# Kernel optimization log

Measured on AMD Instinct MI355X. Metric: run time of the kernel, lower is better.

## Reference

```python
import jax, jax.numpy as jnp
import numpy as np

B, N, G = 8, 512, 16          # images, proposals/img, gt boxes/img
C = 91                        # num classes (incl background)
FEAT = 256 * 7 * 7            # pooled RoI feature dim = 12544
REP = 1024                    # TwoMLPHead representation size
FG, BG = 0.5, 0.5             # fg/bg IoU thresholds
BBOX_W = (10.0, 10.0, 5.0, 5.0)
BETA = 1.0 / 9.0              # smooth-L1 beta


def setup_inputs() -> dict:
    key = jax.random.key(0)
    ks = jax.random.split(key, 12)
    # valid xyxy boxes inside an ~800x800 image
    tl = jax.random.uniform(ks[0], (B, N, 2), minval=0.0, maxval=700.0)
    wh = jax.random.uniform(ks[1], (B, N, 2), minval=8.0, maxval=128.0)
    proposals = jnp.concatenate([tl, tl + wh], axis=-1)
    gtl = jax.random.uniform(ks[2], (B, G, 2), minval=0.0, maxval=700.0)
    gwh = jax.random.uniform(ks[3], (B, G, 2), minval=8.0, maxval=128.0)
    gt_boxes = jnp.concatenate([gtl, gtl + gwh], axis=-1)
    gt_labels = jax.random.randint(ks[4], (B, G), 1, C)  # foreground labels 1..C-1
    P = N + G
    features = jax.random.normal(ks[5], (B * P, FEAT), dtype=jnp.float32)
    s = 0.01
    return {
        'proposals': proposals, 'gt_boxes': gt_boxes, 'features': features,
        'W1': jax.random.normal(ks[6], (FEAT, REP), jnp.float32) * s,
        'b1': jnp.zeros((REP,), jnp.float32),
        'W2': jax.random.normal(ks[7], (REP, REP), jnp.float32) * s,
        'b2': jnp.zeros((REP,), jnp.float32),
        'Wcls': jax.random.normal(ks[8], (REP, C), jnp.float32) * s,
        'bcls': jnp.zeros((C,), jnp.float32),
        'Wbox': jax.random.normal(ks[9], (REP, C * 4), jnp.float32) * s,
        'bbox': jnp.zeros((C * 4,), jnp.float32),
        'gt_labels': gt_labels,
    }


def _box_iou(gt, pr):
    # gt: [B,G,4], pr: [B,P,4] -> [B,G,P]
    area_g = (gt[..., 2] - gt[..., 0]) * (gt[..., 3] - gt[..., 1])
    area_p = (pr[..., 2] - pr[..., 0]) * (pr[..., 3] - pr[..., 1])
    lt = jnp.maximum(gt[:, :, None, :2], pr[:, None, :, :2])
    rb = jnp.minimum(gt[:, :, None, 2:], pr[:, None, :, 2:])
    wh = jnp.clip(rb - lt, 0.0)
    inter = wh[..., 0] * wh[..., 1]
    return inter / (area_g[:, :, None] + area_p[:, None, :] - inter)


def _encode(ref, gt):
    # torchvision BoxCoder.encode_single; ref/gt: [...,4]
    wx, wy, ww, wh = BBOX_W
    ew = ref[..., 2] - ref[..., 0]; eh = ref[..., 3] - ref[..., 1]
    ex = ref[..., 0] + 0.5 * ew;    ey = ref[..., 1] + 0.5 * eh
    gw = gt[..., 2] - gt[..., 0];   gh = gt[..., 3] - gt[..., 1]
    gx = gt[..., 0] + 0.5 * gw;     gy = gt[..., 1] + 0.5 * gh
    return jnp.stack([
        wx * (gx - ex) / ew, wy * (gy - ey) / eh,
        ww * jnp.log(gw / ew), wh * jnp.log(gh / eh)], axis=-1)


def reference(proposals, gt_boxes, features, W1, b1, W2, b2, Wcls, bcls, Wbox, bbox, gt_labels):
    # add_gt_proposals
    props = jnp.concatenate([proposals, gt_boxes], axis=1)  # [B,P,4]
    # assign_targets_to_proposals (Matcher, allow_low_quality_matches=False)
    iou = _box_iou(gt_boxes, props)                          # [B,G,P]
    matched_vals = iou.max(axis=1)                           # [B,P]
    matched_idx = iou.argmax(axis=1)                         # [B,P]
    labels = jnp.take_along_axis(gt_labels, matched_idx, axis=1)
    labels = jnp.where(matched_vals < BG, 0, labels)                         # background
    labels = jnp.where((matched_vals >= BG) & (matched_vals < FG), -1, labels)  # ignore
    matched_gt = jnp.take_along_axis(gt_boxes, matched_idx[..., None], axis=1)  # [B,P,4]
    reg_targets = _encode(props, matched_gt).reshape(-1, 4)  # [R,4]
    labels = labels.reshape(-1)                               # [R]

    # TwoMLPHead + FastRCNNPredictor
    x = jax.nn.relu(features @ W1 + b1)
    x = jax.nn.relu(x @ W2 + b2)
    class_logits = x @ Wcls + bcls                            # [R,C]
    box_regression = (x @ Wbox + bbox).reshape(-1, C, 4)      # [R,C,4]

    # fastrcnn_loss (all proposals; ignored labels (-1) masked from CE)
    R = class_logits.shape[0]
    valid = (labels >= 0).astype(class_logits.dtype)
    safe_lab = jnp.clip(labels, 0, C - 1)
    logp = jax.nn.log_softmax(class_logits, axis=-1)
    nll = -jnp.take_along_axis(logp, safe_lab[:, None], axis=1)[:, 0]
    classification_loss = (nll * valid).sum() / jnp.maximum(valid.sum(), 1.0)

    pos = (labels > 0).astype(class_logits.dtype)
    pred = jnp.take_along_axis(box_regression, safe_lab[:, None, None], axis=1)[:, 0]  # [R,4]
    d = jnp.abs(pred - reg_targets)
    sl1 = jnp.where(d < BETA, 0.5 * d * d / BETA, d - 0.5 * BETA).sum(-1)
    box_loss = (sl1 * pos).sum() / R

    return jnp.stack([classification_loss, box_loss])
```

## Files before the change

kernel.cpp:

```cpp
#include <hip/hip_runtime.h>
#include <cstdint>
#include <cstddef>

#define BQ   8
#define NP   512
#define GQ   16
#define PP   528
#define RT   4224
#define MPAD 4352
#define CC   91
#define FEATD 12544
#define REPD 1024
#define NH   512
#define NHU  455
#define BETA (1.0f/9.0f)
#define WSC  64.0f

typedef float f32x4 __attribute__((ext_vector_type(4)));
typedef int   v8i  __attribute__((ext_vector_type(8)));
typedef float v16f __attribute__((ext_vector_type(16)));

__device__ __forceinline__ unsigned short f2bf(float f) {
  unsigned int x = __float_as_uint(f);
  unsigned int r = (x + 0x7fffu + ((x >> 16) & 1u)) >> 16;
  return (unsigned short)r;
}
__device__ __forceinline__ float bf2f(unsigned short u) {
  return __uint_as_float((unsigned int)u << 16);
}

__device__ __forceinline__ void ld_lds16(const void* g, void* l) {
  __builtin_amdgcn_global_load_lds(
      (const __attribute__((address_space(1))) void*)g,
      (__attribute__((address_space(3))) void*)l, 16, 0, 0);
}

__device__ __forceinline__ size_t img_off(int row, int kb, int KT) {
  return (size_t)((row >> 7) * KT + (kb >> 6)) * 8192
       + (size_t)((((row >> 5) & 3) << 11) + (((kb >> 4) & 3) << 9)
                  + ((row & 31) << 4) + (kb & 15));
}

constexpr size_t O_W1T = 0;
constexpr size_t SZ_W1T = (size_t)FEATD * REPD;
constexpr size_t O_W2T = O_W1T + SZ_W1T;
constexpr size_t SZ_W2T = (size_t)REPD * REPD;
constexpr size_t O_WH  = O_W2T + SZ_W2T;
constexpr size_t SZ_WH = (size_t)NH * REPD;
constexpr size_t O_BH  = O_WH + SZ_WH;
constexpr size_t SZ_BH = (size_t)NH * 4;
constexpr size_t O_X1  = O_BH + SZ_BH;
constexpr size_t SZ_X1 = (size_t)MPAD * REPD;
constexpr size_t O_X2  = O_X1 + SZ_X1;
constexpr size_t O_LAB = O_X2 + SZ_X1;
constexpr size_t O_TGT = O_LAB + (size_t)RT * 4;
constexpr size_t O_NLL = O_TGT + (size_t)RT * 16;
constexpr size_t O_VC  = O_NLL + (size_t)RT * 4;
constexpr size_t O_SL1 = O_VC + (size_t)RT * 4;
constexpr size_t O_PART = ((O_SL1 + (size_t)RT * 4) + 255) & ~(size_t)255;
constexpr size_t SZ_PART = (size_t)4 * MPAD * REPD * 2;
constexpr size_t O_F8 = O_PART + SZ_PART;

#define NB_CV ((MPAD/32)*(FEATD/256))
__global__ void prep_cv(const float* __restrict__ feat, unsigned char* __restrict__ feat8) {
  __shared__ unsigned char lb[32 * 264];
  const int b = blockIdx.x, t = threadIdx.x;
  const int yb = b / (FEATD / 256), kc4 = b % (FEATD / 256);
  const int w = t >> 6, L = t & 63;
  const int row0 = yb * 32;
  if (row0 < RT) {
#pragma unroll
    for (int i = 0; i < 8; ++i) {
      int r = w * 8 + i;
      float4 f = *(const float4*)(feat + (size_t)(row0 + r) * FEATD + kc4 * 256 + L * 4);
      unsigned int pk = (unsigned int)__builtin_amdgcn_cvt_pk_fp8_f32(f.x, f.y, 0, false);
      pk = (unsigned int)__builtin_amdgcn_cvt_pk_fp8_f32(f.z, f.w, (int)pk, true);
      *(unsigned int*)&lb[r * 264 + L * 4] = pk;
    }
  } else {
#pragma unroll
    for (int i = 0; i < 8; ++i)
      *(unsigned int*)&lb[(w * 8 + i) * 264 + L * 4] = 0u;
  }
  __syncthreads();
  const size_t base = ((size_t)(yb >> 2) * (FEATD / 64) + kc4 * 4) * 8192
                    + (size_t)(yb & 3) * 2048;
#pragma unroll
  for (int q = 0; q < 2; ++q) {
    int s = t + 256 * q;
    int tile = s >> 7, kc = (s >> 5) & 3, r = s & 31;
    int4 v = *(const int4*)&lb[r * 264 + tile * 64 + kc * 16];
    *(int4*)&feat8[base + (size_t)tile * 8192 + kc * 512 + r * 16] = v;
  }
}

__device__ __forceinline__ void tr128(const float* __restrict__ in, unsigned char* __restrict__ out,
                                      int K, int N, int row_off, int KT,
                                      int bx, int by, int t, float (*tile)[36]) {
  const int n0 = bx * 32, k0 = by * 128;
  const int n4 = t & 7, kr = t >> 3;
  if (n0 + 32 <= N) {
#pragma unroll
    for (int i = 0; i < 4; ++i) {
      int k = k0 + kr + i * 32;
      float4 f = *(const float4*)&in[(size_t)k * N + n0 + n4 * 4];
      *(float4*)&tile[kr + i * 32][n4 * 4] = f;
    }
  } else {
#pragma unroll
    for (int i = 0; i < 4; ++i) {
      int k = k0 + kr + i * 32;
#pragma unroll
      for (int j = 0; j < 4; ++j) {
        int n = n0 + n4 * 4 + j;
        tile[kr + i * 32][n4 * 4 + j] = (n < N) ? in[(size_t)k * N + n] : 0.0f;
      }
    }
  }
  __syncthreads();
  const int rn = t & 31, kc = t >> 5;
  const int n = n0 + rn;
  if (n < N) {
    unsigned int pk[4];
#pragma unroll
    for (int q = 0; q < 4; ++q) {
      float f0 = tile[kc * 16 + q * 4 + 0][rn] * WSC;
      float f1 = tile[kc * 16 + q * 4 + 1][rn] * WSC;
      float f2 = tile[kc * 16 + q * 4 + 2][rn] * WSC;
      float f3 = tile[kc * 16 + q * 4 + 3][rn] * WSC;
      unsigned int r = (unsigned int)__builtin_amdgcn_cvt_pk_fp8_f32(f0, f1, 0, false);
      pk[q] = (unsigned int)__builtin_amdgcn_cvt_pk_fp8_f32(f2, f3, (int)r, true);
    }
    int4 v; v.x = (int)pk[0]; v.y = (int)pk[1]; v.z = (int)pk[2]; v.w = (int)pk[3];
    *(int4*)&out[img_off(n + row_off, k0 + kc * 16, KT)] = v;
  }
}

#define NBW1 ((REPD/32)*(FEATD/128))
#define NBW2 ((REPD/32)*(REPD/128))
#define NBWC (3*(REPD/128))
#define NBWB (12*(REPD/128))
#define NB_PW (NBW1+NBW2+NBWC+NBWB)

__global__ void prep_w(const float* __restrict__ W1, const float* __restrict__ W2,
                       const float* __restrict__ Wcls, const float* __restrict__ Wbox,
                       unsigned char* __restrict__ W1t, unsigned char* __restrict__ W2t,
                       unsigned char* __restrict__ Wh) {
  __shared__ float tile[128][36];
  int b = blockIdx.x, t = threadIdx.x;
  if (b < NBW1) { tr128(W1, W1t, FEATD, REPD, 0, FEATD/64, b % 32, b / 32, t, tile); return; }
  b -= NBW1;
  if (b < NBW2) { tr128(W2, W2t, REPD, REPD, 0, REPD/64, b % 32, b / 32, t, tile); return; }
  b -= NBW2;
  if (b < NBWC) { tr128(Wcls, Wh, REPD, CC, 0, REPD/64, b % 3, b / 3, t, tile); return; }
  b -= NBWC;
  tr128(Wbox, Wh, REPD, 4 * CC, CC, REPD/64, b % 12, b / 12, t, tile);
}

#define NB_HI 230
#define NB_MT 17
#define NB_MISC (NB_HI+NB_MT)
__global__ void prep_misc(const float* __restrict__ bcls, const float* __restrict__ bbox,
                          const float* __restrict__ proposals, const float* __restrict__ gt_boxes,
                          const int* __restrict__ gt_labels,
                          unsigned char* __restrict__ Wh, float* __restrict__ bh,
                          int* __restrict__ labels, float* __restrict__ tgts) {
  int b = blockIdx.x, t = threadIdx.x;
  if (b < NB_HI) {
    int idx = b * 256 + t;
    const int npad = (NH - NHU) * REPD;
    if (idx < npad) {
      int row = NHU + (idx >> 10), k = idx & 1023;
      Wh[img_off(row, k, REPD/64)] = 0;
    } else {
      int i2 = idx - npad;
      if (i2 < NH) bh[i2] = (i2 < CC) ? bcls[i2] : (i2 < NHU ? bbox[i2 - CC] : 0.0f);
    }
    return;
  }
  b -= NB_HI;
  int r = b * 256 + t;
  if (r >= RT) return;
  int bi_ = r / PP, p = r % PP;
  float x0, y0, x1, y1;
  if (p < NP) {
    const float* qq = proposals + ((size_t)bi_ * NP + p) * 4;
    x0 = qq[0]; y0 = qq[1]; x1 = qq[2]; y1 = qq[3];
  } else {
    const float* qq = gt_boxes + ((size_t)bi_ * GQ + (p - NP)) * 4;
    x0 = qq[0]; y0 = qq[1]; x1 = qq[2]; y1 = qq[3];
  }
  float ap = (x1 - x0) * (y1 - y0);
  float best = -1.0f; int bg = 0;
#pragma unroll
  for (int g = 0; g < GQ; ++g) {
    const float* gb = gt_boxes + ((size_t)bi_ * GQ + g) * 4;
    float gx0 = gb[0], gy0 = gb[1], gx1 = gb[2], gy1 = gb[3];
    float ag = (gx1 - gx0) * (gy1 - gy0);
    float iw = fmaxf(fminf(gx1, x1) - fmaxf(gx0, x0), 0.0f);
    float ih = fmaxf(fminf(gy1, y1) - fmaxf(gy0, y0), 0.0f);
    float inter = iw * ih;
    float iou = inter / (ag + ap - inter);
    if (iou > best) { best = iou; bg = g; }
  }
  int lab = gt_labels[bi_ * GQ + bg];
  if (best < 0.5f) lab = 0;
  labels[r] = lab;
  const float* gb = gt_boxes + ((size_t)bi_ * GQ + bg) * 4;
  float ew = x1 - x0, eh = y1 - y0;
  float ex = x0 + 0.5f * ew, ey = y0 + 0.5f * eh;
  float gw = gb[2] - gb[0], gh = gb[3] - gb[1];
  float gx = gb[0] + 0.5f * gw, gy = gb[1] + 0.5f * gh;
  tgts[r * 4 + 0] = 10.0f * (gx - ex) / ew;
  tgts[r * 4 + 1] = 10.0f * (gy - ey) / eh;
  tgts[r * 4 + 2] = 5.0f * logf(gw / ew);
  tgts[r * 4 + 3] = 5.0f * logf(gh / eh);
}

__global__ __launch_bounds__(256, 4)
void gemm_f8(const unsigned char* __restrict__ Aimg, const unsigned char* __restrict__ Bimg,
             unsigned short* __restrict__ P, int Mp, int Nc, int KT, int nkt,
             int n_nblk, int n_my, int npairs) {
  __shared__ unsigned char As[2 * 8192];
  __shared__ unsigned char Bs[2 * 8192];

  const int g = blockIdx.x;
  const int xcd = g & 7;
  const int kix = g >> 3;
  const int n  = kix % n_nblk;
  const int pi = kix / n_nblk;
  const int p  = pi * 8 + xcd;
  if (p >= npairs) return;
  const int y  = p % n_my;
  const int kz = p / n_my;
  const int m0 = y * 128, n0 = n * 128;

  const int tid = threadIdx.x;
  const int w = tid >> 6, L = tid & 63;
  const int l31 = L & 31, h = L >> 5;
  const int wr = (w >> 1) * 64, wc = (w & 1) * 64;

  const int kt0 = kz * nkt;
  const unsigned char* gA = Aimg + ((size_t)y * KT + kt0) * 8192 + w * 2048 + L * 16;
  const unsigned char* gB = Bimg + ((size_t)n * KT + kt0) * 8192 + w * 2048 + L * 16;
  const int lw = w * 2048;

#define STAGE(it, bufo) do {                                    \
    const size_t _go = (size_t)(it) * 8192;                     \
    ld_lds16(gA + _go,        &As[(bufo) + lw]);                \
    ld_lds16(gA + _go + 1024, &As[(bufo) + lw + 1024]);         \
    ld_lds16(gB + _go,        &Bs[(bufo) + lw]);                \
    ld_lds16(gB + _go + 1024, &Bs[(bufo) + lw + 1024]);         \
  } while (0)

  int aoff[2], boff[2];
#pragma unroll
  for (int i = 0; i < 2; ++i) {
    aoff[i] = (((w >> 1) * 2 + i) << 11) + (h << 10) + (l31 << 4);
    boff[i] = (((w & 1) * 2 + i) << 11) + (h << 10) + (l31 << 4);
  }

  STAGE(0, 0);

  v16f acc[2][2] = {};
  int cur = 0;
  for (int it = 0; it < nkt; ++it) {
    const int cb = cur << 13;
    if (it + 1 < nkt) {
      STAGE(it + 1, cb ^ 8192);
      asm volatile("s_waitcnt vmcnt(4)" ::: "memory");
    } else {
      asm volatile("s_waitcnt vmcnt(0)" ::: "memory");
    }
    __builtin_amdgcn_sched_barrier(0);
    __builtin_amdgcn_s_barrier();

    v8i a[2], b[2];
#pragma unroll
    for (int i = 0; i < 2; ++i) {
      int4 alo = *(const int4*)&As[cb + aoff[i]];
      int4 ahi = *(const int4*)&As[cb + aoff[i] + 512];
      a[i] = (v8i){alo.x, alo.y, alo.z, alo.w, ahi.x, ahi.y, ahi.z, ahi.w};
      int4 blo = *(const int4*)&Bs[cb + boff[i]];
      int4 bhi = *(const int4*)&Bs[cb + boff[i] + 512];
      b[i] = (v8i){blo.x, blo.y, blo.z, blo.w, bhi.x, bhi.y, bhi.z, bhi.w};
    }
#pragma unroll
    for (int i = 0; i < 2; ++i)
#pragma unroll
      for (int j = 0; j < 2; ++j)
        acc[i][j] = __builtin_amdgcn_mfma_scale_f32_32x32x64_f8f6f4(
            a[i], b[j], acc[i][j], 0, 0, 0, 127, 0, 127);

    asm volatile("s_waitcnt lgkmcnt(0)" ::: "memory");
    __builtin_amdgcn_sched_barrier(0);
    __builtin_amdgcn_s_barrier();
    cur ^= 1;
  }
#undef STAGE

  unsigned short* Pz = P + (size_t)kz * Mp * Nc;
#pragma unroll
  for (int i = 0; i < 2; ++i) {
#pragma unroll
    for (int j = 0; j < 2; ++j) {
      int colb = n0 + wc + j * 32 + l31;
#pragma unroll
      for (int r = 0; r < 16; ++r) {
        int row = m0 + wr + i * 32 + (r & 3) + 8 * (r >> 2) + 4 * h;
        Pz[(size_t)row * Nc + colb] = f2bf(acc[i][j][r]);
      }
    }
  }
}

template <int S>
__global__ void reduce_fp8k(const unsigned short* __restrict__ P, const float* __restrict__ bias,
                            unsigned int* __restrict__ outp, long MN4, int nc4) {
  long i = (long)blockIdx.x * blockDim.x + threadIdx.x;
  long stride = (long)gridDim.x * blockDim.x;
  const ushort4* P4 = (const ushort4*)P;
  const float4* B4 = (const float4*)bias;
  for (; i < MN4; i += stride) {
    float vx = 0, vy = 0, vz = 0, vw = 0;
#pragma unroll
    for (int s = 0; s < S; ++s) {
      ushort4 u = P4[s * MN4 + i];
      vx += bf2f(u.x); vy += bf2f(u.y); vz += bf2f(u.z); vw += bf2f(u.w);
    }
    float4 b = B4[i & (nc4 - 1)];
    vx = fmaxf(vx * (1.0f / WSC) + b.x, 0.0f);
    vy = fmaxf(vy * (1.0f / WSC) + b.y, 0.0f);
    vz = fmaxf(vz * (1.0f / WSC) + b.z, 0.0f);
    vw = fmaxf(vw * (1.0f / WSC) + b.w, 0.0f);
    unsigned int r = (unsigned int)__builtin_amdgcn_cvt_pk_fp8_f32(vx, vy, 0, false);
    r = (unsigned int)__builtin_amdgcn_cvt_pk_fp8_f32(vz, vw, (int)r, true);
    int rr = (int)(i >> 8);
    int kb = ((int)i & 255) * 4;
    outp[img_off(rr, kb, REPD / 64) >> 2] = r;
  }
}

__global__ void loss_row(const unsigned short* __restrict__ P, const float* __restrict__ bh,
                         const int* __restrict__ labels, const float* __restrict__ tgts,
                         float* __restrict__ nll_v, float* __restrict__ vc_v,
                         float* __restrict__ sl1_v) {
  int r = blockIdx.x;
  int l = threadIdx.x;
  const size_t SL = (size_t)MPAD * NH;
  const unsigned short* p0 = P + (size_t)r * NH;
#define COLV(c) ((bf2f(p0[(c)]) + bf2f(p0[SL + (c)]) + bf2f(p0[2 * SL + (c)]) + \
                  bf2f(p0[3 * SL + (c)])) * (1.0f / WSC) + bh[(c)])
  float v1 = COLV(l);
  float v2 = (l < CC - 64) ? COLV(64 + l) : -3.4e38f;
  float m = fmaxf(v1, v2);
#pragma unroll
  for (int o = 32; o; o >>= 1) m = fmaxf(m, __shfl_xor(m, o));
  float e = __expf(v1 - m) + ((l < CC - 64) ? __expf(v2 - m) : 0.0f);
#pragma unroll
  for (int o = 32; o; o >>= 1) e += __shfl_xor(e, o);
  if (l == 0) {
    float lse = m + __logf(e);
    int lab = labels[r];
    int sl = lab < 0 ? 0 : (lab > CC - 1 ? CC - 1 : lab);
    float valid = (lab >= 0) ? 1.0f : 0.0f;
    nll_v[r] = (lse - COLV(sl)) * valid;
    vc_v[r] = valid;
    float s = 0.0f;
#pragma unroll
    for (int d = 0; d < 4; ++d) {
      float pd = COLV(CC + sl * 4 + d);
      float ad = fabsf(pd - tgts[r * 4 + d]);
      s += (ad < BETA) ? 0.5f * ad * ad / BETA : ad - 0.5f * BETA;
    }
    sl1_v[r] = (lab > 0) ? s : 0.0f;
  }
#undef COLV
}

__global__ void reduce_final(const float* __restrict__ nll_v, const float* __restrict__ vc_v,
                             const float* __restrict__ sl1_v, float* __restrict__ out) {
  __shared__ float s1[256], s2[256], s3[256];
  int t = threadIdx.x;
  float a = 0, b = 0, c = 0;
  for (int i = t; i < RT; i += 256) { a += nll_v[i]; b += vc_v[i]; c += sl1_v[i]; }
  s1[t] = a; s2[t] = b; s3[t] = c;
  __syncthreads();
  for (int o = 128; o; o >>= 1) {
    if (t < o) { s1[t] += s1[t + o]; s2[t] += s2[t + o]; s3[t] += s3[t + o]; }
    __syncthreads();
  }
  if (t == 0) {
    out[0] = s1[0] / fmaxf(s2[0], 1.0f);
    out[1] = s3[0] / (float)RT;
  }
}

extern "C" void kernel_launch(void* const* d_in, const int* in_sizes, int n_in,
                              void* d_out, int out_size, void* d_ws, size_t ws_size,
                              hipStream_t stream) {
  const float* proposals = (const float*)d_in[0];
  const float* gt_boxes  = (const float*)d_in[1];
  const float* features  = (const float*)d_in[2];
  const float* W1   = (const float*)d_in[3];
  const float* b1   = (const float*)d_in[4];
  const float* W2   = (const float*)d_in[5];
  const float* b2   = (const float*)d_in[6];
  const float* Wcls = (const float*)d_in[7];
  const float* bcls = (const float*)d_in[8];
  const float* Wbox = (const float*)d_in[9];
  const float* bbox = (const float*)d_in[10];
  const int* gt_labels = (const int*)d_in[11];
  float* out = (float*)d_out;

  char* ws = (char*)d_ws;
  unsigned char* W1t = (unsigned char*)(ws + O_W1T);
  unsigned char* W2t = (unsigned char*)(ws + O_W2T);
  unsigned char* Wh  = (unsigned char*)(ws + O_WH);
  float* bh          = (float*)(ws + O_BH);
  unsigned char* x1  = (unsigned char*)(ws + O_X1);
  unsigned char* x2  = (unsigned char*)(ws + O_X2);
  int* labels        = (int*)(ws + O_LAB);
  float* tgts        = (float*)(ws + O_TGT);
  float* nll_v       = (float*)(ws + O_NLL);
  float* vc_v        = (float*)(ws + O_VC);
  float* sl1_v       = (float*)(ws + O_SL1);
  unsigned short* part = (unsigned short*)(ws + O_PART);
  unsigned char* feat8 = (unsigned char*)(ws + O_F8);

  prep_cv<<<NB_CV, 256, 0, stream>>>(features, feat8);
  prep_w<<<NB_PW, 256, 0, stream>>>(W1, W2, Wcls, Wbox, W1t, W2t, Wh);
  prep_misc<<<NB_MISC, 256, 0, stream>>>(bcls, bbox, proposals, gt_boxes, gt_labels,
                                         Wh, bh, labels, tgts);

  gemm_f8<<<1088, 256, 0, stream>>>(feat8, W1t, part, MPAD, REPD, FEATD/64, 49,
                                    8, 34, 136);
  reduce_fp8k<4><<<2048, 256, 0, stream>>>(part, b1, (unsigned int*)x1,
                                           (long)MPAD * REPD / 4, REPD / 4);

  gemm_f8<<<576, 256, 0, stream>>>(x1, W2t, part, MPAD, REPD, REPD/64, 8,
                                   8, 34, 68);
  reduce_fp8k<2><<<2048, 256, 0, stream>>>(part, b2, (unsigned int*)x2,
                                           (long)MPAD * REPD / 4, REPD / 4);

  gemm_f8<<<544, 256, 0, stream>>>(x2, Wh, part, MPAD, NH, REPD/64, 4,
                                   4, 34, 136);

  loss_row<<<RT, 64, 0, stream>>>(part, bh, labels, tgts, nll_v, vc_v, sl1_v);
  reduce_final<<<1, 256, 0, stream>>>(nll_v, vc_v, sl1_v, out);
}
```

Before: 476.4 us.

## Widen FP8 GEMM block tile to 128x256 with 8 waves per block

Each gemm_f8 block now computes a 128x256 output tile using 512 threads (8 waves in a 2x4 layout), staging two B column blocks per k-step. A tiles are reused across twice as many columns, and the grid sizes are halved to match. The second GEMM also switches from 2-way to 4-way split-K (8 iterations per slice become 4), with the reduction updated to sum 4 partials. This trades fewer A reloads for more LDS per block and possibly lower occupancy, plus more partial-sum traffic in the second layer.

```diff
diff --git a/kernel.cpp b/kernel.cpp
--- a/kernel.cpp
+++ b/kernel.cpp
@@ -217,12 +217,12 @@
   tgts[r * 4 + 3] = 5.0f * logf(gh / eh);
 }
 
-__global__ __launch_bounds__(256, 4)
+__global__ __launch_bounds__(512, 4)
 void gemm_f8(const unsigned char* __restrict__ Aimg, const unsigned char* __restrict__ Bimg,
              unsigned short* __restrict__ P, int Mp, int Nc, int KT, int nkt,
              int n_nblk, int n_my, int npairs) {
   __shared__ unsigned char As[2 * 8192];
-  __shared__ unsigned char Bs[2 * 8192];
+  __shared__ unsigned char Bs[2 * 16384];
 
   const int g = blockIdx.x;
   const int xcd = g & 7;
@@ -233,42 +233,46 @@
   if (p >= npairs) return;
   const int y  = p % n_my;
   const int kz = p / n_my;
-  const int m0 = y * 128, n0 = n * 128;
+  const int m0 = y * 128, n0 = n * 256;
 
   const int tid = threadIdx.x;
   const int w = tid >> 6, L = tid & 63;
   const int l31 = L & 31, h = L >> 5;
-  const int wr = (w >> 1) * 64, wc = (w & 1) * 64;
+  const int mw = w >> 2, nw = w & 3;
 
   const int kt0 = kz * nkt;
-  const unsigned char* gA = Aimg + ((size_t)y * KT + kt0) * 8192 + w * 2048 + L * 16;
-  const unsigned char* gB = Bimg + ((size_t)n * KT + kt0) * 8192 + w * 2048 + L * 16;
-  const int lw = w * 2048;
-
-#define STAGE(it, bufo) do {                                    \
+  const unsigned char* gA  = Aimg + ((size_t)y * KT + kt0) * 8192 + w * 1024 + L * 16;
+  const unsigned char* gB0 = Bimg + ((size_t)(2 * n) * KT + kt0) * 8192 + w * 1024 + L * 16;
+  const unsigned char* gB1 = Bimg + ((size_t)(2 * n + 1) * KT + kt0) * 8192 + w * 1024 + L * 16;
+  const int lwA = w * 1024;
+  const int lwB0 = w * 1024, lwB1 = 8192 + w * 1024;
+
+#define STAGE(it, ba, bb) do {                                  \
     const size_t _go = (size_t)(it) * 8192;                     \
-    ld_lds16(gA + _go,        &As[(bufo) + lw]);                \
-    ld_lds16(gA + _go + 1024, &As[(bufo) + lw + 1024]);         \
-    ld_lds16(gB + _go,        &Bs[(bufo) + lw]);                \
-    ld_lds16(gB + _go + 1024, &Bs[(bufo) + lw + 1024]);         \
+    ld_lds16(gA  + _go, &As[(ba) + lwA]);                       \
+    ld_lds16(gB0 + _go, &Bs[(bb) + lwB0]);                      \
+    ld_lds16(gB1 + _go, &Bs[(bb) + lwB1]);                      \
   } while (0)
 
   int aoff[2], boff[2];
 #pragma unroll
-  for (int i = 0; i < 2; ++i) {
-    aoff[i] = (((w >> 1) * 2 + i) << 11) + (h << 10) + (l31 << 4);
-    boff[i] = (((w & 1) * 2 + i) << 11) + (h << 10) + (l31 << 4);
-  }
-
-  STAGE(0, 0);
+  for (int i = 0; i < 2; ++i)
+    aoff[i] = ((mw * 2 + i) << 11) + (h << 10) + (l31 << 4);
+#pragma unroll
+  for (int j = 0; j < 2; ++j) {
+    int c5 = nw * 2 + j;
+    boff[j] = (c5 >> 2) * 8192 + ((c5 & 3) << 11) + (h << 10) + (l31 << 4);
+  }
+
+  STAGE(0, 0, 0);
 
   v16f acc[2][2] = {};
   int cur = 0;
   for (int it = 0; it < nkt; ++it) {
-    const int cb = cur << 13;
+    const int ba = cur * 8192, bb = cur * 16384;
     if (it + 1 < nkt) {
-      STAGE(it + 1, cb ^ 8192);
-      asm volatile("s_waitcnt vmcnt(4)" ::: "memory");
+      STAGE(it + 1, ba ^ 8192, bb ^ 16384);
+      asm volatile("s_waitcnt vmcnt(3)" ::: "memory");
     } else {
       asm volatile("s_waitcnt vmcnt(0)" ::: "memory");
     }
@@ -278,11 +282,11 @@
     v8i a[2], b[2];
 #pragma unroll
     for (int i = 0; i < 2; ++i) {
-      int4 alo = *(const int4*)&As[cb + aoff[i]];
-      int4 ahi = *(const int4*)&As[cb + aoff[i] + 512];
+      int4 alo = *(const int4*)&As[ba + aoff[i]];
+      int4 ahi = *(const int4*)&As[ba + aoff[i] + 512];
       a[i] = (v8i){alo.x, alo.y, alo.z, alo.w, ahi.x, ahi.y, ahi.z, ahi.w};
-      int4 blo = *(const int4*)&Bs[cb + boff[i]];
-      int4 bhi = *(const int4*)&Bs[cb + boff[i] + 512];
+      int4 blo = *(const int4*)&Bs[bb + boff[i]];
+      int4 bhi = *(const int4*)&Bs[bb + boff[i] + 512];
       b[i] = (v8i){blo.x, blo.y, blo.z, blo.w, bhi.x, bhi.y, bhi.z, bhi.w};
     }
 #pragma unroll
@@ -304,10 +308,10 @@
   for (int i = 0; i < 2; ++i) {
 #pragma unroll
     for (int j = 0; j < 2; ++j) {
-      int colb = n0 + wc + j * 32 + l31;
+      int colb = n0 + nw * 64 + j * 32 + l31;
 #pragma unroll
       for (int r = 0; r < 16; ++r) {
-        int row = m0 + wr + i * 32 + (r & 3) + 8 * (r >> 2) + 4 * h;
+        int row = m0 + mw * 64 + i * 32 + (r & 3) + 8 * (r >> 2) + 4 * h;
         Pz[(size_t)row * Nc + colb] = f2bf(acc[i][j][r]);
       }
     }
@@ -433,18 +437,18 @@
   prep_misc<<<NB_MISC, 256, 0, stream>>>(bcls, bbox, proposals, gt_boxes, gt_labels,
                                          Wh, bh, labels, tgts);
 
-  gemm_f8<<<1088, 256, 0, stream>>>(feat8, W1t, part, MPAD, REPD, FEATD/64, 49,
-                                    8, 34, 136);
+  gemm_f8<<<544, 512, 0, stream>>>(feat8, W1t, part, MPAD, REPD, FEATD/64, 49,
+                                   4, 34, 136);
   reduce_fp8k<4><<<2048, 256, 0, stream>>>(part, b1, (unsigned int*)x1,
                                            (long)MPAD * REPD / 4, REPD / 4);
 
-  gemm_f8<<<576, 256, 0, stream>>>(x1, W2t, part, MPAD, REPD, REPD/64, 8,
-                                   8, 34, 68);
-  reduce_fp8k<2><<<2048, 256, 0, stream>>>(part, b2, (unsigned int*)x2,
+  gemm_f8<<<544, 512, 0, stream>>>(x1, W2t, part, MPAD, REPD, REPD/64, 4,
+                                   4, 34, 136);
+  reduce_fp8k<4><<<2048, 256, 0, stream>>>(part, b2, (unsigned int*)x2,
                                            (long)MPAD * REPD / 4, REPD / 4);
 
-  gemm_f8<<<544, 256, 0, stream>>>(x2, Wh, part, MPAD, NH, REPD/64, 4,
-                                   4, 34, 136);
+  gemm_f8<<<272, 512, 0, stream>>>(x2, Wh, part, MPAD, NH, REPD/64, 4,
+                                   2, 34, 136);
 
   loss_row<<<RT, 64, 0, stream>>>(part, bh, labels, tgts, nll_v, vc_v, sl1_v);
   reduce_final<<<1, 256, 0, stream>>>(nll_v, vc_v, sl1_v, out);
```

Measured after the change: 505.0 us. +6.0%, slower.
